# Optimization experiments

Measured on AMD Instinct MI355X. Metric: run time of the kernel, lower is better.

Reference implementation:

```python
import jax, jax.numpy as jnp
import numpy as np

K = 5          # kernel_size
PAD = (K - 1) // 2  # fixed_padding with dilation=1, stride=1 -> 'same'


def setup_inputs() -> dict:
    key = jax.random.key(0)
    kx, kw = jax.random.split(key)
    x = jax.random.normal(kx, (4, 8, 512, 512), dtype=jnp.float32)
    # nn.Parameter initialized to zeros in the original; use small random values
    # so the op is non-trivial (math is identical for any weight values).
    weight = jax.random.normal(kw, (8, 8, K, K), dtype=jnp.float32) * 0.05
    return {"x": x, "weight": weight}


def reference(x, weight):
    """Morphological dilation2d with hard max (soft_max=False).

    out[n,o,h,w] = max_{c,dy,dx} ( x_pad[n,c,h+dy,w+dx] + weight[o,c,dy,dx] )
    Faithful to: pad zeros -> unfold -> weight + x -> max over dim C*k*k.
    Computed as a fused sliding-window max-plus reduction (no (N,C,k,k,H,W)
    unfold tensor is materialized; loop is over the fixed k*k kernel taps).
    """
    N, C, H, W = x.shape
    O = weight.shape[0]
    xp = jnp.pad(x, ((0, 0), (0, 0), (PAD, PAD), (PAD, PAD)))  # zero pad, as in F.pad
    out = jnp.full((N, O, H, W), -jnp.inf, dtype=x.dtype)
    for dy in range(K):
        for dx in range(K):
            patch = xp[:, :, dy:dy + H, dx:dx + W]           # (N,C,H,W)
            w_tap = weight[:, :, dy, dx]                      # (O,C)
            # (N,1,C,H,W) + (1,O,C,1,1) -> max over C -> (N,O,H,W)
            term = patch[:, None] + w_tap[None, :, :, None, None]
            out = jnp.maximum(out, jnp.max(term, axis=2))
    return out
```

## Files before the change

### kernel.cpp

```cpp
#include <hip/hip_runtime.h>
#include <math.h>
#include <stdint.h>

#define KK 5
#define PADK 2
#define C_IN 8
#define O_OUT 8
#define HH 512
#define WW 512
#define TH 8
#define TW 128
#define CH 4
#define LROWS 12
#define LCOLS 136
#define WSTR 12
#define NW (O_OUT * C_IN * KK * KK)
#define XHALF (CH * LROWS * (LCOLS / 2))

static __device__ __forceinline__ float max3f(float a, float b, float c) {
    float d;
    asm("v_max3_f32 %0, %1, %2, %3" : "=v"(d) : "v"(a), "v"(b), "v"(c));
    return d;
}

__global__ __launch_bounds__(512, 8)
void dil_kernel(const float* __restrict__ x,
                const float* __restrict__ wf,
                float* __restrict__ out) {
    __shared__ __align__(16) float xlds[CH][LROWS][LCOLS];
    __shared__ __align__(16) float wlds[C_IN * KK * 4 * WSTR];

    const int tid = threadIdx.x;
    const int w0 = blockIdx.x * TW;
    const int h0 = blockIdx.y * TH;
    const int n  = blockIdx.z;
    const float* xn = x + (size_t)n * (C_IN * HH * WW);

    const int l   = tid & 63;
    const int wid = tid >> 6;

    float acc[O_OUT][2];
    #pragma unroll
    for (int o = 0; o < O_OUT; ++o) {
        acc[o][0] = -INFINITY;
        acc[o][1] = -INFINITY;
    }

    for (int h = 0; h < 2; ++h) {
        if (h) __syncthreads();

        for (int idx = tid; idx < XHALF; idx += 512) {
            int cc  = idx / (LROWS * (LCOLS / 2));
            int rem = idx - cc * (LROWS * (LCOLS / 2));
            int r   = rem / (LCOLS / 2);
            int jp  = rem - r * (LCOLS / 2);
            int gh = h0 - PADK + r;
            int gw = w0 - PADK + 2 * jp;
            float v0 = 0.f, v1 = 0.f;
            if ((unsigned)gh < (unsigned)HH) {
                const float* row = xn + ((size_t)(h * CH + cc) * HH + gh) * WW;
                if ((unsigned)gw < (unsigned)WW) v0 = row[gw];
                if ((unsigned)(gw + 1) < (unsigned)WW) v1 = row[gw + 1];
            }
            *(float2*)&xlds[cc][r][2 * jp] = make_float2(v0, v1);
        }
        if (h == 0) {
            for (int t = tid; t < NW; t += 512) {
                int dx = t % KK;  int q = t / KK;
                int o2 = q & 1;   q >>= 1;
                int dy = q % KK;  q /= KK;
                int g  = q & 3;   int c = q >> 2;
                int o = g * 2 + o2;
                wlds[((c * KK + dy) * 4 + g) * WSTR + o2 * KK + dx] =
                    wf[((o * C_IN + c) * KK + dy) * KK + dx];
            }
        }
        __syncthreads();

        for (int cc = 0; cc < CH; ++cc) {
            const int c = h * CH + cc;
            #pragma unroll
            for (int dy = 0; dy < KK; ++dy) {
                const float* lr = &xlds[cc][wid + dy][2 * l];
                float2 a = *(const float2*)(lr);
                float2 b = *(const float2*)(lr + 2);
                float2 d = *(const float2*)(lr + 4);
                const float u0 = a.x, u1 = a.y, u2 = b.x,
                            u3 = b.y, u4 = d.x, u5 = d.y;
                const float* wdy = &wlds[(c * KK + dy) * 4 * WSTR];
                #pragma unroll
                for (int g = 0; g < 4; ++g) {
                    const float* wch = wdy + g * WSTR;
                    float4 wa = *(const float4*)(wch);
                    float4 wv = *(const float4*)(wch + 4);
                    float2 wc2 = *(const float2*)(wch + 8);
                    const float w[10] = {wa.x, wa.y, wa.z, wa.w,
                                         wv.x, wv.y, wv.z, wv.w,
                                         wc2.x, wc2.y};
                    #pragma unroll
                    for (int o2 = 0; o2 < 2; ++o2) {
                        const int o = g * 2 + o2;
                        const float* wo = &w[o2 * 5];
                        float t0 = u0 + wo[0], t1 = u1 + wo[1],
                              t2 = u2 + wo[2], t3 = u3 + wo[3],
                              t4 = u4 + wo[4];
                        acc[o][0] = max3f(acc[o][0],
                                          max3f(t0, t1, t2),
                                          fmaxf(t3, t4));
                        float s0 = u1 + wo[0], s1 = u2 + wo[1],
                              s2 = u3 + wo[2], s3 = u4 + wo[3],
                              s4 = u5 + wo[4];
                        acc[o][1] = max3f(acc[o][1],
                                          max3f(s0, s1, s2),
                                          fmaxf(s3, s4));
                    }
                }
            }
        }
    }

    float* onp = out + (size_t)n * (O_OUT * HH * WW);
    const int hB = h0 + wid;
    const int wcol = w0 + 2 * l;
    #pragma unroll
    for (int o = 0; o < O_OUT; ++o) {
        float2 rr = make_float2(acc[o][0], acc[o][1]);
        *(float2*)(&onp[((size_t)o * HH + hB) * WW + wcol]) = rr;
    }
}

extern "C" void kernel_launch(void* const* d_in, const int* in_sizes, int n_in,
                              void* d_out, int out_size, void* d_ws, size_t ws_size,
                              hipStream_t stream) {
    const float* x   = (const float*)d_in[0];
    const float* wgt = (const float*)d_in[1];
    float* out = (float*)d_out;

    dim3 grid(WW / TW, HH / TH, 4);
    dim3 block(512);
    dil_kernel<<<grid, block, 0, stream>>>(x, wgt, out);
}
```

Baseline: 67.54 us.

## Compute four output columns per thread and enlarge row tile

Each thread now produces four adjacent output pixels instead of two, and the block tile doubles in height. Input channels are staged in four phases of two channels. This reuses LDS input and weight loads across more outputs and reduces halo overhead, at the cost of more accumulator registers, a lower occupancy bound, and more barriers per block.

```diff
diff --git a/kernel.cpp b/kernel.cpp
--- a/kernel.cpp
+++ b/kernel.cpp
@@ -8,14 +8,14 @@
 #define O_OUT 8
 #define HH 512
 #define WW 512
-#define TH 8
+#define TH 16
 #define TW 128
-#define CH 4
-#define LROWS 12
+#define CH 2
+#define LROWS 20
 #define LCOLS 136
 #define WSTR 12
 #define NW (O_OUT * C_IN * KK * KK)
-#define XHALF (CH * LROWS * (LCOLS / 2))
+#define XQ (CH * LROWS * (LCOLS / 2))
 
 static __device__ __forceinline__ float max3f(float a, float b, float c) {
     float d;
@@ -23,7 +23,7 @@
     return d;
 }
 
-__global__ __launch_bounds__(512, 8)
+__global__ __launch_bounds__(512, 4)
 void dil_kernel(const float* __restrict__ x,
                 const float* __restrict__ wf,
                 float* __restrict__ out) {
@@ -37,19 +37,21 @@
     const float* xn = x + (size_t)n * (C_IN * HH * WW);
 
     const int l   = tid & 63;
+    const int s   = l & 31;
+    const int hw  = l >> 5;
     const int wid = tid >> 6;
+    const int loc = wid * 2 + hw;
 
-    float acc[O_OUT][2];
+    float acc[O_OUT][4];
     #pragma unroll
-    for (int o = 0; o < O_OUT; ++o) {
-        acc[o][0] = -INFINITY;
-        acc[o][1] = -INFINITY;
-    }
+    for (int o = 0; o < O_OUT; ++o)
+        #pragma unroll
+        for (int p = 0; p < 4; ++p) acc[o][p] = -INFINITY;
 
-    for (int h = 0; h < 2; ++h) {
-        if (h) __syncthreads();
+    for (int ph = 0; ph < C_IN / CH; ++ph) {
+        if (ph) __syncthreads();
 
-        for (int idx = tid; idx < XHALF; idx += 512) {
+        for (int idx = tid; idx < XQ; idx += 512) {
             int cc  = idx / (LROWS * (LCOLS / 2));
             int rem = idx - cc * (LROWS * (LCOLS / 2));
             int r   = rem / (LCOLS / 2);
@@ -58,13 +60,13 @@
             int gw = w0 - PADK + 2 * jp;
             float v0 = 0.f, v1 = 0.f;
             if ((unsigned)gh < (unsigned)HH) {
-                const float* row = xn + ((size_t)(h * CH + cc) * HH + gh) * WW;
+                const float* row = xn + ((size_t)(ph * CH + cc) * HH + gh) * WW;
                 if ((unsigned)gw < (unsigned)WW) v0 = row[gw];
                 if ((unsigned)(gw + 1) < (unsigned)WW) v1 = row[gw + 1];
             }
             *(float2*)&xlds[cc][r][2 * jp] = make_float2(v0, v1);
         }
-        if (h == 0) {
+        if (ph == 0) {
             for (int t = tid; t < NW; t += 512) {
                 int dx = t % KK;  int q = t / KK;
                 int o2 = q & 1;   q >>= 1;
@@ -78,41 +80,38 @@
         __syncthreads();
 
         for (int cc = 0; cc < CH; ++cc) {
-            const int c = h * CH + cc;
+            const int c = ph * CH + cc;
             #pragma unroll
             for (int dy = 0; dy < KK; ++dy) {
-                const float* lr = &xlds[cc][wid + dy][2 * l];
-                float2 a = *(const float2*)(lr);
-                float2 b = *(const float2*)(lr + 2);
-                float2 d = *(const float2*)(lr + 4);
-                const float u0 = a.x, u1 = a.y, u2 = b.x,
-                            u3 = b.y, u4 = d.x, u5 = d.y;
+                const float* lr = &xlds[cc][loc + dy][4 * s];
+                float4 A = *(const float4*)(lr);
+                float4 B = *(const float4*)(lr + 4);
+                const float u[8] = {A.x, A.y, A.z, A.w, B.x, B.y, B.z, B.w};
                 const float* wdy = &wlds[(c * KK + dy) * 4 * WSTR];
                 #pragma unroll
-                for (int g = 0; g < 4; ++g) {
-                    const float* wch = wdy + g * WSTR;
+                for (int og = 0; og < 4; ++og) {
+                    const float* wch = wdy + og * WSTR;
                     float4 wa = *(const float4*)(wch);
-                    float4 wv = *(const float4*)(wch + 4);
+                    float4 wb = *(const float4*)(wch + 4);
                     float2 wc2 = *(const float2*)(wch + 8);
                     const float w[10] = {wa.x, wa.y, wa.z, wa.w,
-                                         wv.x, wv.y, wv.z, wv.w,
+                                         wb.x, wb.y, wb.z, wb.w,
                                          wc2.x, wc2.y};
                     #pragma unroll
                     for (int o2 = 0; o2 < 2; ++o2) {
-                        const int o = g * 2 + o2;
+                        const int o = og * 2 + o2;
                         const float* wo = &w[o2 * 5];
-                        float t0 = u0 + wo[0], t1 = u1 + wo[1],
-                              t2 = u2 + wo[2], t3 = u3 + wo[3],
-                              t4 = u4 + wo[4];
-                        acc[o][0] = max3f(acc[o][0],
-                                          max3f(t0, t1, t2),
-                                          fmaxf(t3, t4));
-                        float s0 = u1 + wo[0], s1 = u2 + wo[1],
-                              s2 = u3 + wo[2], s3 = u4 + wo[3],
-                              s4 = u5 + wo[4];
-                        acc[o][1] = max3f(acc[o][1],
-                                          max3f(s0, s1, s2),
-                                          fmaxf(s3, s4));
+                        #pragma unroll
+                        for (int p = 0; p < 4; ++p) {
+                            float t0 = u[p + 0] + wo[0];
+                            float t1 = u[p + 1] + wo[1];
+                            float t2 = u[p + 2] + wo[2];
+                            float t3 = u[p + 3] + wo[3];
+                            float t4 = u[p + 4] + wo[4];
+                            acc[o][p] = max3f(acc[o][p],
+                                              max3f(t0, t1, t2),
+                                              fmaxf(t3, t4));
+                        }
                     }
                 }
             }
@@ -120,12 +119,12 @@
     }
 
     float* onp = out + (size_t)n * (O_OUT * HH * WW);
-    const int hB = h0 + wid;
-    const int wcol = w0 + 2 * l;
+    const int h = h0 + loc;
+    const int col = w0 + 4 * s;
     #pragma unroll
     for (int o = 0; o < O_OUT; ++o) {
-        float2 rr = make_float2(acc[o][0], acc[o][1]);
-        *(float2*)(&onp[((size_t)o * HH + hB) * WW + wcol]) = rr;
+        float4 rr = make_float4(acc[o][0], acc[o][1], acc[o][2], acc[o][3]);
+        *(float4*)(&onp[((size_t)o * HH + h) * WW + col]) = rr;
     }
 }
 
```

Result: no change. 67.04 us (-0.7%).
